# Kernel optimization log

Measured on AMD Instinct MI355X. Metric: run time of the kernel, lower is better.

The kernel has to match this reference:

```python
import jax, jax.numpy as jnp
import numpy as np

B, C_IN, H, W = 8, 64, 128, 128
C_OUT = 64
K = 3            # kernel size
STRIDE, PAD, DIL, DG = 1, 1, 1, 1
CIN2 = C_IN + 2  # coord channels appended
KK = K * K
CH_OM = DG * 3 * KK  # 27 offset/mask channels


def setup_inputs() -> dict:
    key = jax.random.key(0)
    k1, k2, k3, k4 = jax.random.split(key, 4)
    stdv = 1.0 / np.sqrt(CIN2 * K * K)
    return {
        "input": jax.random.normal(k1, (B, C_IN, H, W), jnp.float32),
        "weight": jax.random.uniform(k2, (C_OUT, CIN2, K, K), jnp.float32, -stdv, stdv),
        "bias": jnp.zeros((C_OUT,), jnp.float32),
        # torch init is zeros; use small random so offsets/mask are non-trivial
        "w_om": jax.random.normal(k3, (CH_OM, CIN2, K, K), jnp.float32) * 0.01,
        "b_om": jax.random.normal(k4, (CH_OM,), jnp.float32) * 0.01,
    }


def _bilinear(img, ph, pw):
    # img: [Cg, H, W]; ph, pw: [KK, Ho, Wo] float sampling coords
    Hh, Ww = img.shape[-2], img.shape[-1]
    h0 = jnp.floor(ph)
    w0 = jnp.floor(pw)
    lh = ph - h0
    lw = pw - w0
    hh = 1.0 - lh
    hw = 1.0 - lw

    def g(hi, wi):
        ok = ((hi >= 0) & (hi < Hh) & (wi >= 0) & (wi < Ww)).astype(img.dtype)
        hi_c = jnp.clip(hi.astype(jnp.int32), 0, Hh - 1)
        wi_c = jnp.clip(wi.astype(jnp.int32), 0, Ww - 1)
        return img[:, hi_c, wi_c] * ok  # [Cg, KK, Ho, Wo]

    return (g(h0, w0) * (hh * hw) + g(h0, w0 + 1) * (hh * lw)
            + g(h0 + 1, w0) * (lh * hw) + g(h0 + 1, w0 + 1) * (lh * lw))


def reference(input, weight, bias, w_om, b_om):
    b, c, h, w = input.shape
    # coordinate channels (h index normalized, w index normalized and centered)
    h_i = jnp.broadcast_to((jnp.arange(h, dtype=jnp.float32) / h)[:, None], (h, w))
    w_i = jnp.broadcast_to((jnp.arange(w, dtype=jnp.float32) / w - 0.5)[None, :], (h, w))
    im_i = jnp.stack([h_i, w_i], 0)  # [2, h, w]
    x = jnp.concatenate([input, jnp.broadcast_to(im_i[None], (b, 2, h, w))], axis=1)

    # offset/mask prediction conv
    om = jax.lax.conv_general_dilated(
        x, w_om, (STRIDE, STRIDE), [(PAD, PAD), (PAD, PAD)],
        rhs_dilation=(DIL, DIL), dimension_numbers=("NCHW", "OIHW", "NCHW"))
    om = om + b_om[None, :, None, None]
    o1, o2, m = jnp.split(om, 3, axis=1)
    offset = jnp.concatenate([o1, o2], axis=1)   # [b, 2*DG*KK, Ho, Wo]
    mask = jax.nn.sigmoid(m)                     # [b, DG*KK, Ho, Wo]
    Ho, Wo = offset.shape[2], offset.shape[3]

    # CUDA dcn_v2 interprets offset channels as [dg, KK, (h,w)] interleaved
    off = offset.reshape(b, DG, KK, 2, Ho, Wo)
    off_h, off_w = off[:, :, :, 0], off[:, :, :, 1]
    mk = mask.reshape(b, DG, KK, Ho, Wo)

    tap_h = jnp.repeat(jnp.arange(K), K).astype(jnp.float32)  # [KK]
    tap_w = jnp.tile(jnp.arange(K), K).astype(jnp.float32)
    ph = off_h + (tap_h[:, None, None] * DIL
                  + jnp.arange(Ho, dtype=jnp.float32)[None, :, None] * STRIDE - PAD)
    pw = off_w + (tap_w[:, None, None] * DIL
                  + jnp.arange(Wo, dtype=jnp.float32)[None, None, :] * STRIDE - PAD)

    xg = x.reshape(b, DG, CIN2 // DG, h, w)
    # [b, dg, Cg, KK, Ho, Wo] bilinear-sampled columns
    cols = jax.vmap(jax.vmap(_bilinear))(xg, ph, pw)
    cols = cols * mk[:, :, None]
    wr = weight.reshape(C_OUT, DG, CIN2 // DG, KK)
    out = jnp.einsum("ogck,bgckhw->bohw", wr, cols) + bias[None, :, None, None]

    # index_i as in the torch code
    n = DG * KK
    kk = int(np.sqrt(n))
    rng = jnp.arange(-(kk // 2), kk // 2 + 1).astype(jnp.float32)
    kh_i = jnp.repeat(rng, kk)
    kw_i = jnp.tile(rng, kk)
    k_i = jnp.stack([kh_i, kw_i], 0)               # [2, n]
    idx = im_i[:, None] + k_i[:, :, None, None]    # [2, n, h, w]
    idx = jnp.broadcast_to(idx.reshape(1, 2 * n, h, w), (b, 2 * n, Ho, Wo)) + offset
    return out, idx, mask
```

## Files before the change

### kernel.cpp

```cpp
#include <hip/hip_runtime.h>
#include <math.h>

#define HW (128*128)

typedef short short8 __attribute__((ext_vector_type(8)));
typedef float floatx4 __attribute__((ext_vector_type(4)));
typedef unsigned int uintx4 __attribute__((ext_vector_type(4)));
typedef _Float16 half2v __attribute__((ext_vector_type(2)));
typedef _Float16 half8v __attribute__((ext_vector_type(8)));

#define MFMA(a,b,c)   __builtin_amdgcn_mfma_f32_16x16x32_bf16((a),(b),(c),0,0,0)
#define MFMA16(a,b,c) __builtin_amdgcn_mfma_f32_16x16x32_f16((a),(b),(c),0,0,0)

union V16 { uintx4 u; half2v h2[4]; half8v h8; _Float16 h[8]; };

#define WT3_ELEMS   (9*3*4*64*8)
#define WMTA_ELEMS  (19*2*4*16*8)
#define WMT_ELEMS   (594*27)
#define TIN_BYTES   ((size_t)8*HW*64*2)
#define WT3_OFF     TIN_BYTES
#define WMTA_OFF    (WT3_OFF + (size_t)WT3_ELEMS*2)
#define WS_FULL     (WMTA_OFF + (size_t)WMTA_ELEMS*2)
#define WS_MID      ((size_t)WT3_ELEMS*2 + (size_t)WMT_ELEMS*4)

static __device__ __forceinline__ unsigned short f2bf(float x) {
    unsigned u = __float_as_uint(x);
    unsigned r = u + 0x7FFFu + ((u >> 16) & 1u);
    return (unsigned short)(r >> 16);
}

static __device__ __forceinline__ unsigned cvt_pk_bf16(float lo, float hi) {
    unsigned r;
    asm("v_cvt_pk_bf16_f32 %0, %1, %2" : "=v"(r) : "v"(lo), "v"(hi));
    return r;
}

__global__ __launch_bounds__(256) void prep_w16(
    const float* __restrict__ weight, const float* __restrict__ w_om,
    _Float16* __restrict__ wt3, _Float16* __restrict__ wmtA)
{
    int t = blockIdx.x * 256 + threadIdx.x;
    if (t < WT3_ELEMS) {
        int i = t & 7;  int u = t >> 3;
        int o = u & 63; u >>= 6;
        int quad = u & 3; u >>= 2;
        int ks = u % 3, kk = u / 3;
        int c = ks * 32 + quad * 8 + i;
        float v = (c < 66) ? weight[o * 594 + c * 9 + kk] : 0.0f;
        wt3[t] = (_Float16)v;
    } else if (t < WT3_ELEMS + WMTA_ELEMS) {
        int t2 = t - WT3_ELEMS;
        int i = t2 & 7;  int u = t2 >> 3;
        int m15 = u & 15; u >>= 4;
        int quad = u & 3; u >>= 2;
        int n = u & 1;    int kt = u >> 1;
        int o = 16 * n + m15;
        float v = 0.0f;
        if (o < 27) {
            if (kt < 18) {
                int j = kt >> 1, c = (kt & 1) * 32 + quad * 8 + i;
                v = w_om[o * 594 + c * 9 + j];
            } else {
                int q = quad * 8 + i;
                if (q < 18) {
                    int j = q >> 1, c = 64 + (q & 1);
                    v = w_om[o * 594 + c * 9 + j];
                }
            }
        }
        wmtA[t2] = (_Float16)v;
    }
}

__global__ __launch_bounds__(256) void prep_t(
    const float* __restrict__ in, _Float16* __restrict__ t_out)
{
    __shared__ float s[64][129];
    const int y = blockIdx.x, b = blockIdx.y;
    const int tid = threadIdx.x, lane = tid & 63, w = tid >> 6;
    const float* src = in + (size_t)b * 64 * HW + y * 128;
#pragma unroll
    for (int i = 0; i < 16; ++i) {
        int c = w * 16 + i;
        s[c][lane]      = src[(size_t)c * HW + lane];
        s[c][lane + 64] = src[(size_t)c * HW + lane + 64];
    }
    __syncthreads();
    _Float16* dst = t_out + ((size_t)b * HW + (size_t)y * 128) * 64;
#pragma unroll
    for (int it = 0; it < 4; ++it) {
        int idx = it * 256 + tid;
        int x = idx >> 3, g = idx & 7;
        V16 v;
#pragma unroll
        for (int j = 0; j < 8; ++j)
            v.h[j] = (_Float16)s[g * 8 + j][x];
        *(uintx4*)&dst[(size_t)x * 64 + g * 8] = v.u;
    }
}

__global__ __launch_bounds__(256) void prep_w(
    const float* __restrict__ weight, const float* __restrict__ w_om,
    unsigned short* __restrict__ wt3, float* __restrict__ wmt)
{
    int t = blockIdx.x * 256 + threadIdx.x;
    if (t < WT3_ELEMS) {
        int i = t & 7;  int u = t >> 3;
        int o = u & 63; u >>= 6;
        int quad = u & 3; u >>= 2;
        int ks = u % 3, kk = u / 3;
        int c = ks * 32 + quad * 8 + i;
        float v = (c < 66) ? weight[o * 594 + c * 9 + kk] : 0.0f;
        wt3[t] = f2bf(v);
    } else if (t < WT3_ELEMS + WMT_ELEMS) {
        int t2 = t - WT3_ELEMS;
        int oc = t2 % 27, ck = t2 / 27;
        wmt[t2] = w_om[oc * 594 + ck];
    }
}

__global__ __launch_bounds__(256, 2) void dcn_hybrid14(
    const _Float16* __restrict__ t_in,
    const _Float16* __restrict__ wt3h,
    const _Float16* __restrict__ wmtA,
    const float* __restrict__ bias,
    const float* __restrict__ b_om,
    float* __restrict__ out)
{
    __shared__ __align__(16) unsigned short s_tile[5 * 68 * 64];
    __shared__ __align__(16) float s_buf[27 * 65];

    _Float16* s_offh16 = (_Float16*)s_buf;
    _Float16* s_offw16 = (_Float16*)s_buf + 576;
    _Float16* s_mask16 = (_Float16*)s_buf + 1152;

    const int tid  = threadIdx.x;
    const int lane = tid & 63;
    const int w    = tid >> 6;
    const int wu   = __builtin_amdgcn_readfirstlane(w);
    const int m15  = lane & 15;
    const int quad = lane >> 4;

    const int L   = blockIdx.x + 2 * (blockIdx.y + 128 * blockIdx.z);
    const int b   = L & 7;
    const int r   = L >> 3;
    const int ho  = r >> 1;
    const int wo0 = (r & 1) * 64;

    const float invH = 1.0f / 128.0f;

    const int pixL = wu * 16 + m15;
    const int wob  = wo0 + pixL;

    const _Float16* tinb = t_in + (size_t)b * HW * 64;
    const _Float16* tinq = tinb + quad * 8;

    for (int Lt = tid; Lt < 340; Lt += 256) {
        int rt = Lt / 68, ct = Lt - rt * 68;
        int gy = min(max(ho - 2 + rt, 0), 127);
        int gx = min(max(wo0 - 2 + ct, 0), 127);
        const uintx4* src = (const uintx4*)(tinb + ((size_t)gy * 128 + gx) * 64);
        uintx4* dst = (uintx4*)&s_tile[(size_t)Lt * 64];
        int sw = ct & 7;
#pragma unroll
        for (int k = 0; k < 8; ++k)
            dst[k ^ sw] = src[k];
    }

    auto tidx = [&](int rt, int ct, int q) -> int {
        return (((rt * 68 + ct) << 3) + (q ^ (ct & 7))) << 3;
    };
    auto tld = [&](int i) -> uintx4 {
        return *(const uintx4*)&s_tile[i];
    };

    int   tr9[9], tc9[9];
    float ok9[9];
#pragma unroll
    for (int j = 0; j < 9; ++j) {
        int y = ho - 1 + j / 3;
        int x = wob - 1 + j % 3;
        bool ok = ((unsigned)y < 128u) && ((unsigned)x < 128u);
        int yc = min(max(y, 0), 127), xc = min(max(x, 0), 127);
        tr9[j] = yc - (ho - 2);
        tc9[j] = xc - (wo0 - 2);
        ok9[j] = ok ? 1.0f : 0.0f;
    }
    __syncthreads();

    floatx4 a0 = (floatx4){0.f, 0.f, 0.f, 0.f};
    floatx4 a1 = (floatx4){0.f, 0.f, 0.f, 0.f};

#pragma unroll
    for (int j = 0; j < 9; ++j) {
        _Float16 okh = (_Float16)ok9[j];
        half2v okh2 = {okh, okh};
        int i0 = tidx(tr9[j], tc9[j], quad);
        V16 bbA, bbB;
        bbA.u = tld(i0);
        bbB.u = tld(i0 ^ 32);
#pragma unroll
        for (int rr = 0; rr < 4; ++rr) {
            bbA.h2[rr] = bbA.h2[rr] * okh2;
            bbB.h2[rr] = bbB.h2[rr] * okh2;
        }
#pragma unroll
        for (int h = 0; h < 2; ++h) {
            const int kt = j * 2 + h;
            const _Float16* ap = wmtA + (size_t)((kt * 2) * 4 + quad) * 128 + m15 * 8;
            half8v A0 = *(const half8v*)ap;
            half8v A1 = *(const half8v*)(ap + 512);
            a0 = MFMA16(A0, h ? bbB.h8 : bbA.h8, a0);
            a1 = MFMA16(A1, h ? bbB.h8 : bbA.h8, a1);
        }
    }
    {
        V16 bb;
#pragma unroll
        for (int rr = 0; rr < 4; ++rr) {
            float ve = 0.f, vo = 0.f;
            int j = quad * 4 + rr;
            if (j < 9) {
                int y = ho - 1 + j / 3;
                int x = wob - 1 + j % 3;
                bool ok = ((unsigned)y < 128u) && ((unsigned)x < 128u);
                ve = ok ? y * invH : 0.f;
                vo = ok ? (x * invH - 0.5f) : 0.f;
            }
            bb.h2[rr] = (half2v){(_Float16)ve, (_Float16)vo};
        }
        const _Float16* ap = wmtA + (size_t)((18 * 2) * 4 + quad) * 128 + m15 * 8;
        half8v A0 = *(const half8v*)ap;
        half8v A1 = *(const half8v*)(ap + 512);
        a0 = MFMA16(A0, bb.h8, a0);
        a1 = MFMA16(A1, bb.h8, a1);
    }

#pragma unroll
    for (int rr = 0; rr < 4; ++rr) {
        s_buf[(quad * 4 + rr) * 65 + pixL] = a0[rr];
        if (quad * 4 + rr < 11)
            s_buf[(16 + quad * 4 + rr) * 65 + pixL] = a1[rr];
    }
    __syncthreads();

    {
        float* out_idx = out + (size_t)8 * 64 * HW;
        float* out_msk = out_idx + (size_t)8 * 18 * HW;
        const int wo = wo0 + lane;
        const int p  = ho * 128 + wo;
        const float hg = ho * invH;
        const float wg = wo * invH - 0.5f;
        int oc0 = wu * 7;
        int noc = (wu == 3) ? 6 : 7;
        float sv[7];
        for (int t = 0; t < noc; ++t)
            sv[t] = s_buf[(oc0 + t) * 65 + lane];
        __syncthreads();
        for (int t = 0; t < noc; ++t) {
            int oc = oc0 + t;
            float s = b_om[oc] + sv[t];
            if (oc < 9) {
                __builtin_nontemporal_store(hg + (float)(oc / 3 - 1) + s,
                    &out_idx[((size_t)b * 18 + oc) * HW + p]);
                if (oc & 1) s_offw16[(oc >> 1) * 64 + lane] = (_Float16)s;
                else        s_offh16[(oc >> 1) * 64 + lane] = (_Float16)s;
            } else if (oc < 18) {
                __builtin_nontemporal_store(wg + (float)((oc - 9) % 3 - 1) + s,
                    &out_idx[((size_t)b * 18 + oc) * HW + p]);
                if (oc & 1) s_offw16[(oc >> 1) * 64 + lane] = (_Float16)s;
                else        s_offh16[(oc >> 1) * 64 + lane] = (_Float16)s;
            } else {
                float mkv = 1.0f / (1.0f + __expf(-s));
                __builtin_nontemporal_store(mkv,
                    &out_msk[((size_t)b * 9 + (oc - 18)) * HW + p]);
                s_mask16[(oc - 18) * 64 + lane] = (_Float16)mkv;
            }
        }
    }
    __syncthreads();

    floatx4 acc[4];
#pragma unroll
    for (int t = 0; t < 4; ++t) acc[t] = (floatx4){0.f, 0.f, 0.f, 0.f};

    const int hom1 = ho - 1;

#pragma unroll
    for (int kk = 0; kk < 9; ++kk) {
        float offh = (float)s_offh16[kk * 64 + pixL];
        float offw = (float)s_offw16[kk * 64 + pixL];
        float mval = (float)s_mask16[kk * 64 + pixL];

        float ph = offh + (float)(kk / 3) + (float)hom1;
        float pw = offw + (float)(kk % 3) + (float)(wob - 1);
        float h0f = floorf(ph), w0f = floorf(pw);
        int h0 = (int)h0f, w0 = (int)w0f;
        int h1 = h0 + 1, w1 = w0 + 1;
        float lh = ph - h0f, lw = pw - w0f;
        float hh = 1.0f - lh, hwp = 1.0f - lw;
        bool okh0 = (unsigned)h0 < 128u, okh1 = (unsigned)h1 < 128u;
        bool okw0 = (unsigned)w0 < 128u, okw1 = (unsigned)w1 < 128u;
        float w00 = (okh0 && okw0) ? hh * hwp * mval : 0.0f;
        float w01 = (okh0 && okw1) ? hh * lw  * mval : 0.0f;
        float w10 = (okh1 && okw0) ? lh * hwp * mval : 0.0f;
        float w11 = (okh1 && okw1) ? lh * lw  * mval : 0.0f;
        int h0c = min(max(h0, 0), 127), h1c = min(max(h1, 0), 127);
        int w0c = min(max(w0, 0), 127), w1c = min(max(w1, 0), 127);

        int r0 = h0c - (ho - 2), r1 = h1c - (ho - 2);
        int c0 = w0c - (wo0 - 2), c1 = w1c - (wo0 - 2);
        bool intile = ((unsigned)r0 < 5u) && ((unsigned)r1 < 5u)
                   && ((unsigned)c0 < 68u) && ((unsigned)c1 < 68u);

        V16 A00, A01, A10, A11, B00, B01, B10, B11;
        if (__all(intile)) {
            int i00 = tidx(r0, c0, quad), i01 = tidx(r0, c1, quad);
            int i10 = tidx(r1, c0, quad), i11 = tidx(r1, c1, quad);
            A00.u = tld(i00);      A01.u = tld(i01);
            A10.u = tld(i10);      A11.u = tld(i11);
            B00.u = tld(i00 ^ 32); B01.u = tld(i01 ^ 32);
            B10.u = tld(i10 ^ 32); B11.u = tld(i11 ^ 32);
        } else {
            int o00 = h0c * 128 + w0c, o01 = h0c * 128 + w1c;
            int o10 = h1c * 128 + w0c, o11 = h1c * 128 + w1c;
            A00.u = *(const uintx4*)(tinq + (size_t)o00 * 64);
            A01.u = *(const uintx4*)(tinq + (size_t)o01 * 64);
            A10.u = *(const uintx4*)(tinq + (size_t)o10 * 64);
            A11.u = *(const uintx4*)(tinq + (size_t)o11 * 64);
            B00.u = *(const uintx4*)(tinq + (size_t)o00 * 64 + 32);
            B01.u = *(const uintx4*)(tinq + (size_t)o01 * 64 + 32);
            B10.u = *(const uintx4*)(tinq + (size_t)o10 * 64 + 32);
            B11.u = *(const uintx4*)(tinq + (size_t)o11 * 64 + 32);
        }

        _Float16 h00 = (_Float16)w00, h01 = (_Float16)w01;
        _Float16 h10 = (_Float16)w10, h11 = (_Float16)w11;
        half2v W00 = {h00, h00}, W01 = {h01, h01};
        half2v W10 = {h10, h10}, W11 = {h11, h11};

        V16 b0, b1, b2;
#pragma unroll
        for (int rr = 0; rr < 4; ++rr) {
            b0.h2[rr] = A00.h2[rr] * W00 + A01.h2[rr] * W01
                      + A10.h2[rr] * W10 + A11.h2[rr] * W11;
            b1.h2[rr] = B00.h2[rr] * W00 + B01.h2[rr] * W01
                      + B10.h2[rr] * W10 + B11.h2[rr] * W11;
        }
        float c64 = (w00 + w01) * (h0c * invH) + (w10 + w11) * (h1c * invH);
        float c65 = (w00 + w10) * (w0c * invH - 0.5f) + (w01 + w11) * (w1c * invH - 0.5f);
        b2.u = (uintx4){0u, 0u, 0u, 0u};
        if (quad == 0) b2.h2[0] = (half2v){(_Float16)c64, (_Float16)c65};

        const _Float16* w0p = wt3h + (size_t)(kk * 3) * 2048 + quad * 512;
        const _Float16* w1p = w0p + 2048;
        const _Float16* w2p = w0p + 4096;
#pragma unroll
        for (int t = 0; t < 4; ++t) {
            int o8 = (16 * t + m15) * 8;
            half8v A0 = *(const half8v*)&w0p[o8];
            half8v A1 = *(const half8v*)&w1p[o8];
            half8v A2 = *(const half8v*)&w2p[o8];
            acc[t] = MFMA16(A0, b0.h8, acc[t]);
            acc[t] = MFMA16(A1, b1.h8, acc[t]);
            acc[t] = MFMA16(A2, b2.h8, acc[t]);
        }
    }

    {
        const size_t rowbase = (size_t)b * 64 * HW + (size_t)ho * 128 + wo0;
#pragma unroll
        for (int t = 0; t < 4; ++t) {
            __syncthreads();
#pragma unroll
            for (int rr = 0; rr < 4; ++rr)
                s_buf[(quad * 4 + rr) * 65 + pixL] = acc[t][rr];
            __syncthreads();
#pragma unroll
            for (int k = 0; k < 4; ++k) {
                int o = 16 * t + wu * 4 + k;
                float v = s_buf[(wu * 4 + k) * 65 + lane] + bias[o];
                __builtin_nontemporal_store(v, &out[(size_t)o * HW + rowbase + lane]);
            }
        }
    }
}

__global__ __launch_bounds__(256, 4) void dcn_hybrid7(
    const float* __restrict__ input,
    const unsigned short* __restrict__ wt3,
    const float* __restrict__ bias,
    const float* __restrict__ wmt,
    const float* __restrict__ b_om,
    float* __restrict__ out)
{
    __shared__ float s_red[4 * 27 * 64];
    __shared__ float s_offh[9 * 64], s_offw[9 * 64], s_maskf[9 * 64];

    const int tid  = threadIdx.x;
    const int lane = tid & 63;
    const int w    = tid >> 6;
    const int wu   = __builtin_amdgcn_readfirstlane(w);
    const int m15  = lane & 15;
    const int quad = lane >> 4;

    const int L   = blockIdx.x + 2 * (blockIdx.y + 128 * blockIdx.z);
    const int b   = L & 7;
    const int r   = L >> 3;
    const int ho  = r >> 1;
    const int wo0 = (r & 1) * 64;

    const int wo  = wo0 + lane;
    const int p   = ho * 128 + wo;
    const float invH = 1.0f / 128.0f;

    const float* inb = input + (size_t)b * 64 * HW;

    int   a9[9];
    float okf[9], vy[9], vx[9];
#pragma unroll
    for (int j = 0; j < 9; ++j) {
        int y = ho - 1 + j / 3;
        int x = wo - 1 + j % 3;
        bool ok = ((unsigned)y < 128u) && ((unsigned)x < 128u);
        int yc = min(max(y, 0), 127), xc = min(max(x, 0), 127);
        a9[j]  = yc * 128 + xc;
        okf[j] = ok ? 1.0f : 0.0f;
        vy[j]  = ok ? y * invH : 0.0f;
        vx[j]  = ok ? (x * invH - 0.5f) : 0.0f;
    }

    const int nc = (wu < 2) ? 17 : 16;

    float om_part[27];
#pragma unroll
    for (int oc = 0; oc < 27; ++oc) om_part[oc] = 0.0f;

    {
        float va[9], vb[9];
        {
            const float* pc = inb + wu * HW;
#pragma unroll
            for (int j = 0; j < 9; ++j) va[j] = pc[a9[j]] * okf[j];
        }
        for (int i = 0; i < nc; ++i) {
            int c = wu + 4 * i;
            if (i + 1 < nc) {
                int cn = c + 4;
                if (cn < 64) {
                    const float* pc = inb + cn * HW;
#pragma unroll
                    for (int j = 0; j < 9; ++j) vb[j] = pc[a9[j]] * okf[j];
                } else if (cn == 64) {
#pragma unroll
                    for (int j = 0; j < 9; ++j) vb[j] = vy[j];
                } else {
#pragma unroll
                    for (int j = 0; j < 9; ++j) vb[j] = vx[j];
                }
            }
#pragma unroll
            for (int j = 0; j < 9; ++j) {
                const float* wp = wmt + (c * 9 + j) * 27;
#pragma unroll
                for (int oc = 0; oc < 27; ++oc)
                    om_part[oc] = fmaf(va[j], wp[oc], om_part[oc]);
            }
#pragma unroll
            for (int j = 0; j < 9; ++j) va[j] = vb[j];
        }
    }
#pragma unroll
    for (int oc = 0; oc < 27; ++oc)
        s_red[(w * 27 + oc) * 64 + lane] = om_part[oc];
    __syncthreads();

    {
        float* out_idx = out + (size_t)8 * 64 * HW;
        float* out_msk = out_idx + (size_t)8 * 18 * HW;
        const float hg = ho * invH;
        const float wg = wo * invH - 0.5f;
        int oc0 = wu * 7;
        int noc = (wu == 3) ? 6 : 7;
        for (int t = 0; t < noc; ++t) {
            int oc = oc0 + t;
            float s = b_om[oc]
                    + s_red[(0 * 27 + oc) * 64 + lane]
                    + s_red[(1 * 27 + oc) * 64 + lane]
                    + s_red[(2 * 27 + oc) * 64 + lane]
                    + s_red[(3 * 27 + oc) * 64 + lane];
            if (oc < 9) {
                out_idx[((size_t)b * 18 + oc) * HW + p] = hg + (float)(oc / 3 - 1) + s;
                if (oc & 1) s_offw[(oc >> 1) * 64 + lane] = s;
                else        s_offh[(oc >> 1) * 64 + lane] = s;
            } else if (oc < 18) {
                out_idx[((size_t)b * 18 + oc) * HW + p] = wg + (float)((oc - 9) % 3 - 1) + s;
                if (oc & 1) s_offw[(oc >> 1) * 64 + lane] = s;
                else        s_offh[(oc >> 1) * 64 + lane] = s;
            } else {
                float mkv = 1.0f / (1.0f + __expf(-s));
                out_msk[((size_t)b * 9 + (oc - 18)) * HW + p] = mkv;
                s_maskf[(oc - 18) * 64 + lane] = mkv;
            }
        }
    }
    __syncthreads();

    const int pixL = wu * 16 + m15;
    const int wob  = wo0 + pixL;
    const int hom1 = ho - 1;

    floatx4 acc[4];
#pragma unroll
    for (int t = 0; t < 4; ++t) acc[t] = (floatx4){0.f, 0.f, 0.f, 0.f};

    const float* base0 = inb + (size_t)(quad * 8) * HW;
    const float* base1 = base0 + (size_t)32 * HW;

#pragma unroll
    for (int kk = 0; kk < 9; ++kk) {
        float offh = s_offh[kk * 64 + pixL];
        float offw = s_offw[kk * 64 + pixL];
        float mval = s_maskf[kk * 64 + pixL];

        float ph = offh + (float)(kk / 3) + (float)hom1;
        float pw = offw + (float)(kk % 3) + (float)(wob - 1);
        float h0f = floorf(ph), w0f = floorf(pw);
        int h0 = (int)h0f, w0 = (int)w0f;
        int h1 = h0 + 1, w1 = w0 + 1;
        float lh = ph - h0f, lw = pw - w0f;
        float hh = 1.0f - lh, hwp = 1.0f - lw;
        bool okh0 = (unsigned)h0 < 128u, okh1 = (unsigned)h1 < 128u;
        bool okw0 = (unsigned)w0 < 128u, okw1 = (unsigned)w1 < 128u;
        float w00 = (okh0 && okw0) ? hh * hwp * mval : 0.0f;
        float w01 = (okh0 && okw1) ? hh * lw  * mval : 0.0f;
        float w10 = (okh1 && okw0) ? lh * hwp * mval : 0.0f;
        float w11 = (okh1 && okw1) ? lh * lw  * mval : 0.0f;
        int h0c = min(max(h0, 0), 127), h1c = min(max(h1, 0), 127);
        int w0c = min(max(w0, 0), 127), w1c = min(max(w1, 0), 127);
        int o00 = h0c * 128 + w0c, o01 = h0c * 128 + w1c;
        int o10 = h1c * 128 + w0c, o11 = h1c * 128 + w1c;

        unsigned pk0[4], pk1[4];
#pragma unroll
        for (int j = 0; j < 4; ++j) {
            const float* pa = base0 + (size_t)(2 * j) * HW;
            const float* pb = pa + HW;
            float ca = w00 * pa[o00] + w01 * pa[o01] + w10 * pa[o10] + w11 * pa[o11];
            float cb = w00 * pb[o00] + w01 * pb[o01] + w10 * pb[o10] + w11 * pb[o11];
            pk0[j] = cvt_pk_bf16(ca, cb);
            const float* pa1 = base1 + (size_t)(2 * j) * HW;
            const float* pb1 = pa1 + HW;
            float ca1 = w00 * pa1[o00] + w01 * pa1[o01] + w10 * pa1[o10] + w11 * pa1[o11];
            float cb1 = w00 * pb1[o00] + w01 * pb1[o01] + w10 * pb1[o10] + w11 * pb1[o11];
            pk1[j] = cvt_pk_bf16(ca1, cb1);
        }
        union { uintx4 u; short8 s; } b0, b1, b2;
        b0.u = (uintx4){pk0[0], pk0[1], pk0[2], pk0[3]};
        b1.u = (uintx4){pk1[0], pk1[1], pk1[2], pk1[3]};
        float c64 = (w00 + w01) * (h0c * invH) + (w10 + w11) * (h1c * invH);
        float c65 = (w00 + w10) * (w0c * invH - 0.5f) + (w01 + w11) * (w1c * invH - 0.5f);
        unsigned pk2 = (quad == 0) ? cvt_pk_bf16(c64, c65) : 0u;
        b2.u = (uintx4){pk2, 0u, 0u, 0u};

        const unsigned short* w0p = wt3 + (size_t)(kk * 3 + 0) * 2048 + quad * 512;
        const unsigned short* w1p = w0p + 2048;
        const unsigned short* w2p = w0p + 4096;
#pragma unroll
        for (int t = 0; t < 4; ++t) {
            int o8 = (16 * t + m15) * 8;
            short8 A0 = *(const short8*)&w0p[o8];
            short8 A1 = *(const short8*)&w1p[o8];
            short8 A2 = *(const short8*)&w2p[o8];
            acc[t] = MFMA(A0, b0.s, acc[t]);
            acc[t] = MFMA(A1, b1.s, acc[t]);
            acc[t] = MFMA(A2, b2.s, acc[t]);
        }
    }

    {
        size_t pb = (size_t)ho * 128 + wob;
#pragma unroll
        for (int t = 0; t < 4; ++t) {
#pragma unroll
            for (int rr = 0; rr < 4; ++rr) {
                int o = 16 * t + quad * 4 + rr;
                out[((size_t)b * 64 + o) * HW + pb] = acc[t][rr] + bias[o];
            }
        }
    }
}

__global__ __launch_bounds__(256) void dcn_fb(
    const float* __restrict__ input,
    const float* __restrict__ wmain,
    const float* __restrict__ bias,
    const float* __restrict__ wom,
    const float* __restrict__ b_om,
    float* __restrict__ out)
{
    const int wo = blockIdx.x * 64 + threadIdx.x;
    const int ho = blockIdx.y * 4 + threadIdx.y;
    const int b  = blockIdx.z;
    const int p  = ho * 128 + wo;
    const float invH = 1.0f / 128.0f;
    const float* inb = input + (size_t)b * 64 * HW;

    float om[27];
#pragma unroll
    for (int oc = 0; oc < 27; ++oc) om[oc] = b_om[oc];

    for (int c = 0; c < 64; ++c) {
        const float* pc = inb + c * HW;
        float v[9];
#pragma unroll
        for (int kh = 0; kh < 3; ++kh) {
            int y = ho - 1 + kh;
            bool oky = (unsigned)y < 128u;
#pragma unroll
            for (int kw = 0; kw < 3; ++kw) {
                int x = wo - 1 + kw;
                bool ok = oky && ((unsigned)x < 128u);
                v[kh*3+kw] = ok ? pc[y * 128 + x] : 0.0f;
            }
        }
#pragma unroll
        for (int oc = 0; oc < 27; ++oc)
#pragma unroll
            for (int i = 0; i < 9; ++i)
                om[oc] = fmaf(v[i], wom[oc*594 + c*9 + i], om[oc]);
    }
    {
        float v64[9], v65[9];
#pragma unroll
        for (int kh = 0; kh < 3; ++kh) {
            int y = ho - 1 + kh;
            bool oky = (unsigned)y < 128u;
#pragma unroll
            for (int kw = 0; kw < 3; ++kw) {
                int x = wo - 1 + kw;
                bool ok = oky && ((unsigned)x < 128u);
                v64[kh*3+kw] = ok ? y * invH : 0.0f;
                v65[kh*3+kw] = ok ? (x * invH - 0.5f) : 0.0f;
            }
        }
#pragma unroll
        for (int oc = 0; oc < 27; ++oc)
#pragma unroll
            for (int i = 0; i < 9; ++i) {
                om[oc] = fmaf(v64[i], wom[oc*594 + 64*9 + i], om[oc]);
                om[oc] = fmaf(v65[i], wom[oc*594 + 65*9 + i], om[oc]);
            }
    }

    const float hg = ho * invH;
    const float wg = wo * invH - 0.5f;
    float* out_idx = out + (size_t)8 * 64 * HW;
    float* out_msk = out_idx + (size_t)8 * 18 * HW;
#pragma unroll
    for (int cc = 0; cc < 9; ++cc)
        out_idx[((size_t)b*18 + cc)*HW + p] = hg + (float)(cc/3 - 1) + om[cc];
#pragma unroll
    for (int cc = 9; cc < 18; ++cc)
        out_idx[((size_t)b*18 + cc)*HW + p] = wg + (float)((cc-9)%3 - 1) + om[cc];

    float mk[9];
#pragma unroll
    for (int kk = 0; kk < 9; ++kk) {
        mk[kk] = 1.0f / (1.0f + __expf(-om[18+kk]));
        out_msk[((size_t)b*9 + kk)*HW + p] = mk[kk];
    }

    float acc[64];
#pragma unroll
    for (int o = 0; o < 64; ++o) acc[o] = bias[o];

#pragma unroll
    for (int kk = 0; kk < 9; ++kk) {
        float ph = om[2*kk]   + (float)(kk/3) + (float)(ho - 1);
        float pw = om[2*kk+1] + (float)(kk%3) + (float)(wo - 1);
        float h0f = floorf(ph), w0f = floorf(pw);
        int h0 = (int)h0f, w0 = (int)w0f;
        int h1 = h0 + 1, w1 = w0 + 1;
        float lh = ph - h0f, lw = pw - w0f;
        float hh = 1.0f - lh, hwp = 1.0f - lw;
        float m = mk[kk];
        bool okh0 = (unsigned)h0 < 128u, okh1 = (unsigned)h1 < 128u;
        bool okw0 = (unsigned)w0 < 128u, okw1 = (unsigned)w1 < 128u;
        float w00 = (okh0 && okw0) ? hh*hwp*m : 0.0f;
        float w01 = (okh0 && okw1) ? hh*lw*m  : 0.0f;
        float w10 = (okh1 && okw0) ? lh*hwp*m : 0.0f;
        float w11 = (okh1 && okw1) ? lh*lw*m  : 0.0f;
        int h0c = min(max(h0, 0), 127), h1c = min(max(h1, 0), 127);
        int w0c = min(max(w0, 0), 127), w1c = min(max(w1, 0), 127);
        int o00 = h0c*128 + w0c, o01 = h0c*128 + w1c;
        int o10 = h1c*128 + w0c, o11 = h1c*128 + w1c;

        for (int c = 0; c < 64; ++c) {
            const float* pc = inb + c * HW;
            float col = w00*pc[o00] + w01*pc[o01] + w10*pc[o10] + w11*pc[o11];
#pragma unroll
            for (int o = 0; o < 64; ++o)
                acc[o] = fmaf(col, wmain[o*594 + c*9 + kk], acc[o]);
        }
        {
            float y0 = h0c * invH, y1 = h1c * invH;
            float x0 = w0c * invH - 0.5f, x1 = w1c * invH - 0.5f;
            float col64 = (w00 + w01)*y0 + (w10 + w11)*y1;
            float col65 = (w00 + w10)*x0 + (w01 + w11)*x1;
#pragma unroll
            for (int o = 0; o < 64; ++o) {
                acc[o] = fmaf(col64, wmain[o*594 + 64*9 + kk], acc[o]);
                acc[o] = fmaf(col65, wmain[o*594 + 65*9 + kk], acc[o]);
            }
        }
    }

#pragma unroll
    for (int o = 0; o < 64; ++o)
        out[((size_t)b*64 + o)*HW + p] = acc[o];
}

extern "C" void kernel_launch(void* const* d_in, const int* in_sizes, int n_in,
                              void* d_out, int out_size, void* d_ws, size_t ws_size,
                              hipStream_t stream)
{
    const float* input  = (const float*)d_in[0];
    const float* weight = (const float*)d_in[1];
    const float* bias   = (const float*)d_in[2];
    const float* w_om   = (const float*)d_in[3];
    const float* b_om   = (const float*)d_in[4];
    float* out = (float*)d_out;

    if (ws_size >= WS_FULL) {
        _Float16* tin  = (_Float16*)d_ws;
        _Float16* wt3h = (_Float16*)((char*)d_ws + WT3_OFF);
        _Float16* wmtA = (_Float16*)((char*)d_ws + WMTA_OFF);
        int total = WT3_ELEMS + WMTA_ELEMS;
        prep_w16<<<(total + 255) / 256, 256, 0, stream>>>(weight, w_om, wt3h, wmtA);
        prep_t<<<dim3(128, 8), 256, 0, stream>>>(input, tin);
        dim3 grid(2, 128, 8);
        dcn_hybrid14<<<grid, dim3(256, 1, 1), 0, stream>>>(tin, wt3h, wmtA, bias, b_om, out);
    } else if (ws_size >= WS_MID) {
        unsigned short* wt3 = (unsigned short*)d_ws;
        float* wmt = (float*)((char*)d_ws + (size_t)WT3_ELEMS * 2);
        int total = WT3_ELEMS + WMT_ELEMS;
        prep_w<<<(total + 255) / 256, 256, 0, stream>>>(weight, w_om, wt3, wmt);
        dim3 grid(2, 128, 8);
        dcn_hybrid7<<<grid, dim3(256, 1, 1), 0, stream>>>(input, wt3, bias, wmt, b_om, out);
    } else {
        dim3 grid(2, 32, 8);
        dcn_fb<<<grid, dim3(64, 4, 1), 0, stream>>>(input, weight, bias, w_om, b_om, out);
    }
}
```

Baseline: 147.9 us.

## Distribute bilinear tap setup across quad lanes and share via ds_bpermute

```diff
diff --git a/kernel.cpp b/kernel.cpp
--- a/kernel.cpp
+++ b/kernel.cpp
@@ -9,10 +9,11 @@
 typedef _Float16 half2v __attribute__((ext_vector_type(2)));
 typedef _Float16 half8v __attribute__((ext_vector_type(8)));
 
+#define MFMA16(a,b,c) __builtin_amdgcn_mfma_f32_16x16x32_f16((a),(b),(c),0,0,0)
 #define MFMA(a,b,c)   __builtin_amdgcn_mfma_f32_16x16x32_bf16((a),(b),(c),0,0,0)
-#define MFMA16(a,b,c) __builtin_amdgcn_mfma_f32_16x16x32_f16((a),(b),(c),0,0,0)
 
 union V16 { uintx4 u; half2v h2[4]; half8v h8; _Float16 h[8]; };
+union H2U { unsigned u; half2v h2; _Float16 h[2]; unsigned short us[2]; };
 
 #define WT3_ELEMS   (9*3*4*64*8)
 #define WMTA_ELEMS  (19*2*4*16*8)
@@ -33,6 +34,11 @@
     unsigned r;
     asm("v_cvt_pk_bf16_f32 %0, %1, %2" : "=v"(r) : "v"(lo), "v"(hi));
     return r;
+}
+
+static __device__ __forceinline__ unsigned pk_f16(float lo, float hi) {
+    H2U v; v.h[0] = (_Float16)lo; v.h[1] = (_Float16)hi;
+    return v.u;
 }
 
 __global__ __launch_bounds__(256) void prep_w16(
@@ -119,7 +125,7 @@
     }
 }
 
-__global__ __launch_bounds__(256, 2) void dcn_hybrid14(
+__global__ __launch_bounds__(256, 2) void dcn_hybrid15(
     const _Float16* __restrict__ t_in,
     const _Float16* __restrict__ wt3h,
     const _Float16* __restrict__ wmtA,
@@ -280,20 +286,17 @@
     }
     __syncthreads();
 
-    floatx4 acc[4];
-#pragma unroll
-    for (int t = 0; t < 4; ++t) acc[t] = (floatx4){0.f, 0.f, 0.f, 0.f};
-
+    unsigned C0[6], C1[6], C2[6];
     const int hom1 = ho - 1;
 
-#pragma unroll
-    for (int kk = 0; kk < 9; ++kk) {
-        float offh = (float)s_offh16[kk * 64 + pixL];
-        float offw = (float)s_offw16[kk * 64 + pixL];
-        float mval = (float)s_mask16[kk * 64 + pixL];
-
-        float ph = offh + (float)(kk / 3) + (float)hom1;
-        float pw = offw + (float)(kk % 3) + (float)(wob - 1);
+    auto mk_ctx = [&](int t, unsigned* C) {
+        float offh = (float)s_offh16[t * 64 + pixL];
+        float offw = (float)s_offw16[t * 64 + pixL];
+        float mval = (float)s_mask16[t * 64 + pixL];
+        int tdh = (t >= 6) ? 2 : ((t >= 3) ? 1 : 0);
+        int tdw = t - 3 * tdh;
+        float ph = offh + (float)tdh + (float)hom1;
+        float pw = offw + (float)tdw + (float)(wob - 1);
         float h0f = floorf(ph), w0f = floorf(pw);
         int h0 = (int)h0f, w0 = (int)w0f;
         int h1 = h0 + 1, w1 = w0 + 1;
@@ -307,21 +310,100 @@
         float w11 = (okh1 && okw1) ? lh * lw  * mval : 0.0f;
         int h0c = min(max(h0, 0), 127), h1c = min(max(h1, 0), 127);
         int w0c = min(max(w0, 0), 127), w1c = min(max(w1, 0), 127);
-
         int r0 = h0c - (ho - 2), r1 = h1c - (ho - 2);
         int c0 = w0c - (wo0 - 2), c1 = w1c - (wo0 - 2);
-        bool intile = ((unsigned)r0 < 5u) && ((unsigned)r1 < 5u)
-                   && ((unsigned)c0 < 68u) && ((unsigned)c1 < 68u);
-
+        unsigned it = (((unsigned)r0 < 5u) && ((unsigned)r1 < 5u)
+                    && ((unsigned)c0 < 68u) && ((unsigned)c1 < 68u)) ? 1u : 0u;
+        C[0] = pk_f16(w00, w01);
+        C[1] = pk_f16(w10, w11);
+        unsigned b00 = ((unsigned)(r0 * 68 + c0) << 6) & 0xFFFFu;
+        unsigned b01 = ((unsigned)(r0 * 68 + c1) << 6) & 0xFFFFu;
+        unsigned b10 = ((unsigned)(r1 * 68 + c0) << 6) & 0xFFFFu;
+        unsigned b11 = ((unsigned)(r1 * 68 + c1) << 6) & 0xFFFFu;
+        C[2] = b00 | ((unsigned)(c0 & 7) << 16) | (it << 19)
+             | ((unsigned)(r0 & 7) << 20) | ((unsigned)(r1 & 7) << 23);
+        C[3] = b01 | ((unsigned)(c1 & 7) << 16) | ((unsigned)(c0 & 127) << 19);
+        C[4] = b10 | ((unsigned)(c0 & 7) << 16) | ((unsigned)(c1 & 127) << 19);
+        C[5] = b11 | ((unsigned)(c1 & 7) << 16);
+    };
+
+    mk_ctx(quad, C0);
+    mk_ctx(quad + 4, C1);
+    mk_ctx((quad == 0) ? 8 : quad, C2);
+
+    floatx4 acc[4];
+#pragma unroll
+    for (int t = 0; t < 4; ++t) acc[t] = (floatx4){0.f, 0.f, 0.f, 0.f};
+
+#pragma unroll
+    for (int kk = 0; kk < 9; ++kk) {
+        const int srcq = kk & 3;
+        const int addr = (m15 + (srcq << 4)) << 2;
+        unsigned cw0, cw1, K00, K01, K10, K11;
+        if (kk < 4) {
+            cw0 = __builtin_amdgcn_ds_bpermute(addr, (int)C0[0]);
+            cw1 = __builtin_amdgcn_ds_bpermute(addr, (int)C0[1]);
+            K00 = __builtin_amdgcn_ds_bpermute(addr, (int)C0[2]);
+            K01 = __builtin_amdgcn_ds_bpermute(addr, (int)C0[3]);
+            K10 = __builtin_amdgcn_ds_bpermute(addr, (int)C0[4]);
+            K11 = __builtin_amdgcn_ds_bpermute(addr, (int)C0[5]);
+        } else if (kk < 8) {
+            cw0 = __builtin_amdgcn_ds_bpermute(addr, (int)C1[0]);
+            cw1 = __builtin_amdgcn_ds_bpermute(addr, (int)C1[1]);
+            K00 = __builtin_amdgcn_ds_bpermute(addr, (int)C1[2]);
+            K01 = __builtin_amdgcn_ds_bpermute(addr, (int)C1[3]);
+            K10 = __builtin_amdgcn_ds_bpermute(addr, (int)C1[4]);
+            K11 = __builtin_amdgcn_ds_bpermute(addr, (int)C1[5]);
+        } else {
+            cw0 = __builtin_amdgcn_ds_bpermute(addr, (int)C2[0]);
+            cw1 = __builtin_amdgcn_ds_bpermute(addr, (int)C2[1]);
+            K00 = __builtin_amdgcn_ds_bpermute(addr, (int)C2[2]);
+            K01 = __builtin_amdgcn_ds_bpermute(addr, (int)C2[3]);
+            K10 = __builtin_amdgcn_ds_bpermute(addr, (int)C2[4]);
+            K11 = __builtin_amdgcn_ds_bpermute(addr, (int)C2[5]);
+        }
+
+        bool it = (K00 >> 19) & 1u;
         V16 A00, A01, A10, A11, B00, B01, B10, B11;
-        if (__all(intile)) {
-            int i00 = tidx(r0, c0, quad), i01 = tidx(r0, c1, quad);
-            int i10 = tidx(r1, c0, quad), i11 = tidx(r1, c1, quad);
+        H2U wab, wcd;
+        float w00f, w01f, w10f, w11f;
+        int h0c, h1c, w0c, w1c;
+
+        if (__all(it)) {
+            int i00 = (int)(K00 & 0xFFFFu) + ((quad ^ (int)((K00 >> 16) & 7)) << 3);
+            int i01 = (int)(K01 & 0xFFFFu) + ((quad ^ (int)((K01 >> 16) & 7)) << 3);
+            int i10 = (int)(K10 & 0xFFFFu) + ((quad ^ (int)((K10 >> 16) & 7)) << 3);
+            int i11 = (int)(K11 & 0xFFFFu) + ((quad ^ (int)((K11 >> 16) & 7)) << 3);
             A00.u = tld(i00);      A01.u = tld(i01);
             A10.u = tld(i10);      A11.u = tld(i11);
             B00.u = tld(i00 ^ 32); B01.u = tld(i01 ^ 32);
             B10.u = tld(i10 ^ 32); B11.u = tld(i11 ^ 32);
+            wab.u = cw0; wcd.u = cw1;
+            w00f = (float)wab.h[0]; w01f = (float)wab.h[1];
+            w10f = (float)wcd.h[0]; w11f = (float)wcd.h[1];
+            int r0 = (int)((K00 >> 20) & 7), r1 = (int)((K00 >> 23) & 7);
+            int c0 = (int)((K01 >> 19) & 127), c1 = (int)((K10 >> 19) & 127);
+            h0c = (ho - 2) + r0; h1c = (ho - 2) + r1;
+            w0c = (wo0 - 2) + c0; w1c = (wo0 - 2) + c1;
         } else {
+            float offh = (float)s_offh16[kk * 64 + pixL];
+            float offw = (float)s_offw16[kk * 64 + pixL];
+            float mval = (float)s_mask16[kk * 64 + pixL];
+            float ph = offh + (float)(kk / 3) + (float)hom1;
+            float pw = offw + (float)(kk % 3) + (float)(wob - 1);
+            float h0f = floorf(ph), w0f = floorf(pw);
+            int h0 = (int)h0f, w0 = (int)w0f;
+            int h1 = h0 + 1, w1 = w0 + 1;
+            float lh = ph - h0f, lw = pw - w0f;
+            float hh = 1.0f - lh, hwp = 1.0f - lw;
+            bool okh0 = (unsigned)h0 < 128u, okh1 = (unsigned)h1 < 128u;
+            bool okw0 = (unsigned)w0 < 128u, okw1 = (unsigned)w1 < 128u;
+            w00f = (okh0 && okw0) ? hh * hwp * mval : 0.0f;
+            w01f = (okh0 && okw1) ? hh * lw  * mval : 0.0f;
+            w10f = (okh1 && okw0) ? lh * hwp * mval : 0.0f;
+            w11f = (okh1 && okw1) ? lh * lw  * mval : 0.0f;
+            h0c = min(max(h0, 0), 127); h1c = min(max(h1, 0), 127);
+            w0c = min(max(w0, 0), 127); w1c = min(max(w1, 0), 127);
             int o00 = h0c * 128 + w0c, o01 = h0c * 128 + w1c;
             int o10 = h1c * 128 + w0c, o11 = h1c * 128 + w1c;
             A00.u = *(const uintx4*)(tinq + (size_t)o00 * 64);
@@ -332,12 +414,12 @@
             B01.u = *(const uintx4*)(tinq + (size_t)o01 * 64 + 32);
             B10.u = *(const uintx4*)(tinq + (size_t)o10 * 64 + 32);
             B11.u = *(const uintx4*)(tinq + (size_t)o11 * 64 + 32);
-        }
-
-        _Float16 h00 = (_Float16)w00, h01 = (_Float16)w01;
-        _Float16 h10 = (_Float16)w10, h11 = (_Float16)w11;
-        half2v W00 = {h00, h00}, W01 = {h01, h01};
-        half2v W10 = {h10, h10}, W11 = {h11, h11};
+            wab.u = pk_f16(w00f, w01f);
+            wcd.u = pk_f16(w10f, w11f);
+        }
+
+        half2v W00 = {wab.h[0], wab.h[0]}, W01 = {wab.h[1], wab.h[1]};
+        half2v W10 = {wcd.h[0], wcd.h[0]}, W11 = {wcd.h[1], wcd.h[1]};
 
         V16 b0, b1, b2;
 #pragma unroll
@@ -347,8 +429,8 @@
             b1.h2[rr] = B00.h2[rr] * W00 + B01.h2[rr] * W01
                       + B10.h2[rr] * W10 + B11.h2[rr] * W11;
         }
-        float c64 = (w00 + w01) * (h0c * invH) + (w10 + w11) * (h1c * invH);
-        float c65 = (w00 + w10) * (w0c * invH - 0.5f) + (w01 + w11) * (w1c * invH - 0.5f);
+        float c64 = (w00f + w01f) * (h0c * invH) + (w10f + w11f) * (h1c * invH);
+        float c65 = (w00f + w10f) * (w0c * invH - 0.5f) + (w01f + w11f) * (w1c * invH - 0.5f);
         b2.u = (uintx4){0u, 0u, 0u, 0u};
         if (quad == 0) b2.h2[0] = (half2v){(_Float16)c64, (_Float16)c65};
 
@@ -740,7 +822,7 @@
         prep_w16<<<(total + 255) / 256, 256, 0, stream>>>(weight, w_om, wt3h, wmtA);
         prep_t<<<dim3(128, 8), 256, 0, stream>>>(input, tin);
         dim3 grid(2, 128, 8);
-        dcn_hybrid14<<<grid, dim3(256, 1, 1), 0, stream>>>(tin, wt3h, wmtA, bias, b_om, out);
+        dcn_hybrid15<<<grid, dim3(256, 1, 1), 0, stream>>>(tin, wt3h, wmtA, bias, b_om, out);
     } else if (ws_size >= WS_MID) {
         unsigned short* wt3 = (unsigned short*)d_ws;
         float* wmt = (float*)((char*)d_ws + (size_t)WT3_ELEMS * 2);
```

Result: no change. 147.8 us (-0.1%).
